# Kernel optimization log

Hardware: AMD Instinct MI355X
Metric: run time of the kernel (lower is better)

The kernel has to match this reference:

```python
import jax, jax.numpy as jnp
import numpy as np
import itertools

N_ELEC = 128
BOX_L = 10.0
DIM = 3
BATCH = 4096


def gen_kpoints(N, L, dim):
    # Faithful numpy port of genKpoints (FermiNet make_kpoints variant).
    rec = 2.0 * np.pi / L
    dk = 1.0 + 1e-05
    max_k = int((N * dk) ** (1.0 / dim) + 0.5)
    ordinals = sorted(range(-max_k, max_k + 1), key=abs)
    ords = np.array(list(itertools.product(ordinals, repeat=dim)), dtype=np.float64)
    kpoints = ords * rec
    order = np.argsort(np.linalg.norm(kpoints, axis=1), kind='stable')
    kpoints = kpoints[order]
    return kpoints[:N].astype(np.float32)


def make_switches(kpoints, dim):
    # Select cos for k-points on the 'positive' side, sin(-k.r) for the rest.
    weights = 10.0 ** np.arange(1, dim + 1)
    weighted_sums = np.sign(kpoints).dot(weights)
    k_signs = np.sign(weighted_sums + 1.0)
    cos_switch = ((k_signs + 1.0) / 2.0).astype(np.float32)
    sin_switch = ((1.0 - k_signs) / 2.0).astype(np.float32)
    return cos_switch, sin_switch


def setup_inputs() -> dict:
    key = jax.random.key(0)
    rs = jax.random.uniform(key, (BATCH, N_ELEC, DIM), dtype=jnp.float32) * BOX_L
    kpoints = gen_kpoints(N_ELEC, BOX_L, DIM)
    cos_switch, sin_switch = make_switches(kpoints, DIM)
    return {
        'rs': rs,
        'kpoints': jnp.asarray(kpoints),
        'cos_switch': jnp.asarray(cos_switch),
        'sin_switch': jnp.asarray(sin_switch),
    }


def reference(rs, kpoints, cos_switch, sin_switch):
    # dots[b, i, m] = k_m . r_{b,i}   -> [B, N, N]
    dots = jnp.einsum('bnd,md->bnm', rs, kpoints)
    # Slater matrix: rows = particles, cols = plane-wave orbitals.
    slater = cos_switch * jnp.cos(dots) + sin_switch * jnp.sin(-dots)
    # log |det| per walker (batched LU) -> [B]
    return jnp.linalg.slogdet(slater)[1]
```

## Files before the change

kernel.cpp:

```cpp
#include <hip/hip_runtime.h>
#include <stdint.h>

#define NM 128
#define NT 512

typedef float v2f __attribute__((ext_vector_type(2)));

__device__ __forceinline__ float readlane_f(float v, int lane) {
    return __int_as_float(__builtin_amdgcn_readlane(__float_as_int(v), lane));
}

__device__ __forceinline__ unsigned wave_max_dpp(unsigned x) {
    int v = (int)x;
#define DPP_STEP(ctrl) \
    { int o = __builtin_amdgcn_update_dpp(0, v, ctrl, 0xf, 0xf, true); \
      v = ((unsigned)o > (unsigned)v) ? o : v; }
    DPP_STEP(0x111)
    DPP_STEP(0x112)
    DPP_STEP(0x114)
    DPP_STEP(0x118)
    DPP_STEP(0x142)
    DPP_STEP(0x143)
#undef DPP_STEP
    return (unsigned)v;
}

__device__ __forceinline__ unsigned pack_key(float v, int r) {
    return (((__float_as_uint(v) & 0x7fffffffu) >> 6) << 7) | (unsigned)r;
}

__device__ __forceinline__ unsigned argmax_bcast(unsigned ka, unsigned kb) {
    const unsigned m = wave_max_dpp(ka > kb ? ka : kb);
    return (unsigned)__builtin_amdgcn_readlane((int)m, 63);
}

__device__ __forceinline__ float sel_readlane(v2f c, int p) {
    return (p < 64) ? readlane_f(c.x, p) : readlane_f(c.y, p - 64);
}

__device__ __forceinline__ void applyBoth(v2f (&sv)[16], int p, v2f lmn) {
    float u[8];
    if (p < 64) {
#pragma unroll
        for (int j = 0; j < 8; ++j) u[j] = readlane_f(sv[j].x, p);
#pragma unroll
        for (int j = 0; j < 8; ++j)
            sv[j] = __builtin_elementwise_fma((v2f){u[j], u[j]}, lmn, sv[j]);
#pragma unroll
        for (int j = 0; j < 8; ++j) u[j] = readlane_f(sv[8 + j].x, p);
#pragma unroll
        for (int j = 0; j < 8; ++j)
            sv[8 + j] = __builtin_elementwise_fma((v2f){u[j], u[j]}, lmn, sv[8 + j]);
    } else {
        const int q = p - 64;
#pragma unroll
        for (int j = 0; j < 8; ++j) u[j] = readlane_f(sv[j].y, q);
#pragma unroll
        for (int j = 0; j < 8; ++j)
            sv[j] = __builtin_elementwise_fma((v2f){u[j], u[j]}, lmn, sv[j]);
#pragma unroll
        for (int j = 0; j < 8; ++j) u[j] = readlane_f(sv[8 + j].y, q);
#pragma unroll
        for (int j = 0; j < 8; ++j)
            sv[8 + j] = __builtin_elementwise_fma((v2f){u[j], u[j]}, lmn, sv[8 + j]);
    }
}

__device__ __forceinline__ void applyHi(v2f (&sv)[16], int p, v2f lmn) {
    float u[8];
    if (p < 64) {
#pragma unroll
        for (int j = 0; j < 8; ++j) u[j] = readlane_f(sv[8 + j].x, p);
#pragma unroll
        for (int j = 0; j < 8; ++j)
            sv[8 + j] = __builtin_elementwise_fma((v2f){u[j], u[j]}, lmn, sv[8 + j]);
    } else {
        const int q = p - 64;
#pragma unroll
        for (int j = 0; j < 8; ++j) u[j] = readlane_f(sv[8 + j].y, q);
#pragma unroll
        for (int j = 0; j < 8; ++j)
            sv[8 + j] = __builtin_elementwise_fma((v2f){u[j], u[j]}, lmn, sv[8 + j]);
    }
}

template<int B>
__device__ __forceinline__ void lookahead8(v2f (&sv)[16], bool& elim0, bool& elim1,
                                           int r0, int r1, int l, int g,
                                           float2 (*colvg)[64],
                                           unsigned* keysF, float* pivsF,
                                           ulonglong2* masks) {
    const bool e0in = elim0, e1in = elim1;
    __builtin_amdgcn_s_setprio(1);
#pragma unroll
    for (int i = 0; i < 8; ++i) {
        const v2f c = sv[B + i];
        const unsigned key = argmax_bcast(elim0 ? 0u : pack_key(c.x, r0),
                                          elim1 ? 0u : pack_key(c.y, r1));
        const int pu = __builtin_amdgcn_readfirstlane((int)(key & 127u));
        const float piv = sel_readlane(c, pu);
        const float rcpn = -__builtin_amdgcn_rcpf(piv);
        elim0 = elim0 || (r0 == pu);
        elim1 = elim1 || (r1 == pu);
        const v2f lmn = { elim0 ? 0.0f : c.x * rcpn,
                          elim1 ? 0.0f : c.y * rcpn };
        colvg[i][l] = make_float2(lmn.x, lmn.y);
        float u[8];
        if (pu < 64) {
#pragma unroll
            for (int m = i + 1; m < 8; ++m) u[m] = readlane_f(sv[B + m].x, pu);
        } else {
#pragma unroll
            for (int m = i + 1; m < 8; ++m) u[m] = readlane_f(sv[B + m].y, pu - 64);
        }
#pragma unroll
        for (int m = i + 1; m < 8; ++m)
            sv[B + m] = __builtin_elementwise_fma((v2f){u[m], u[m]}, lmn, sv[B + m]);
        if (l == 0) { keysF[8 * g + i] = key; pivsF[8 * g + i] = piv; }
    }
    __builtin_amdgcn_s_setprio(0);
    const unsigned long long b0 = __ballot(elim0 && !e0in);
    const unsigned long long b1 = __ballot(elim1 && !e1in);
    if (l == 0) masks[g] = make_ulonglong2(b0, b1);
}

__global__ __launch_bounds__(NT, 8)
void slater_logdet(const float* __restrict__ rs,
                   const float* __restrict__ kpts,
                   const float* __restrict__ csw,
                   const float* __restrict__ ssw,
                   float* __restrict__ out) {
    __shared__ float2 colv[2][8][64];
    __shared__ unsigned keysF[NM];
    __shared__ float    pivsF[NM];
    __shared__ ulonglong2 masks[NM / 8];
    __shared__ float    redf[2];

    const int t  = threadIdx.x;
    const int b  = blockIdx.x;
    const int w  = t >> 6;
    const int l  = t & 63;
    const int r0 = l, r1 = l + 64;

    v2f sv[16];
    {
        const float x0 = rs[(b * NM + r0) * 3 + 0];
        const float y0 = rs[(b * NM + r0) * 3 + 1];
        const float z0 = rs[(b * NM + r0) * 3 + 2];
        const float x1 = rs[(b * NM + r1) * 3 + 0];
        const float y1 = rs[(b * NM + r1) * 3 + 1];
        const float z1 = rs[(b * NM + r1) * 3 + 2];
#pragma unroll
        for (int j = 0; j < 16; ++j) {
            const int m = (j < 8) ? (8 * w + j) : (64 + 8 * w + (j - 8));
            const float kx = kpts[m * 3 + 0], ky = kpts[m * 3 + 1], kz = kpts[m * 3 + 2];
            const float cw = csw[m], sw = ssw[m];
            float sn, cn;
            __sincosf(kx * x0 + ky * y0 + kz * z0, &sn, &cn);
            sv[j].x = cw * cn - sw * sn;
            __sincosf(kx * x1 + ky * y1 + kz * z1, &sn, &cn);
            sv[j].y = cw * cn - sw * sn;
        }
    }

    bool elim0 = false, elim1 = false;

    if (w == 0)
        lookahead8<0>(sv, elim0, elim1, r0, r1, l, 0, colv[0], keysF, pivsF, masks);
    __syncthreads();

    const int liveEnd = w + 7;
    int rd = 0;
    for (; rd <= liveEnd; ++rd) {
        const uint4 ka = *(const uint4*)&keysF[8 * rd];
        const uint4 kb = *(const uint4*)&keysF[8 * rd + 4];
        int p[8];
        p[0] = __builtin_amdgcn_readfirstlane((int)(ka.x & 127u));
        p[1] = __builtin_amdgcn_readfirstlane((int)(ka.y & 127u));
        p[2] = __builtin_amdgcn_readfirstlane((int)(ka.z & 127u));
        p[3] = __builtin_amdgcn_readfirstlane((int)(ka.w & 127u));
        p[4] = __builtin_amdgcn_readfirstlane((int)(kb.x & 127u));
        p[5] = __builtin_amdgcn_readfirstlane((int)(kb.y & 127u));
        p[6] = __builtin_amdgcn_readfirstlane((int)(kb.z & 127u));
        p[7] = __builtin_amdgcn_readfirstlane((int)(kb.w & 127u));
        const ulonglong2 mk = masks[rd];
        elim0 = elim0 || (((mk.x >> l) & 1ull) != 0);
        elim1 = elim1 || (((mk.y >> l) & 1ull) != 0);

        const int par = rd & 1;
        if (rd < w) {
#pragma unroll
            for (int i = 0; i < 8; ++i) {
                const float2 la = colv[par][i][l];
                applyBoth(sv, p[i], (v2f){la.x, la.y});
            }
        } else {
#pragma unroll
            for (int i = 0; i < 8; ++i) {
                const float2 la = colv[par][i][l];
                applyHi(sv, p[i], (v2f){la.x, la.y});
            }
        }

        if (rd == w - 1)
            lookahead8<0>(sv, elim0, elim1, r0, r1, l, rd + 1,
                          colv[(rd + 1) & 1], keysF, pivsF, masks);
        if (rd == w + 7)
            lookahead8<8>(sv, elim0, elim1, r0, r1, l, rd + 1,
                          colv[(rd + 1) & 1], keysF, pivsF, masks);

        __syncthreads();
    }
    for (; rd < 15; ++rd) __syncthreads();

    float lg = 0.0f;
    if (t < NM) {
        lg = __logf(fabsf(pivsF[t]));
#pragma unroll
        for (int off = 32; off > 0; off >>= 1)
            lg += __shfl_xor(lg, off, 64);
        if ((t & 63) == 0) redf[t >> 6] = lg;
    }
    __syncthreads();
    if (t == 0) out[b] = redf[0] + redf[1];
}

extern "C" void kernel_launch(void* const* d_in, const int* in_sizes, int n_in,
                              void* d_out, int out_size, void* d_ws, size_t ws_size,
                              hipStream_t stream) {
    const float* rs = (const float*)d_in[0];
    const float* kp = (const float*)d_in[1];
    const float* cs = (const float*)d_in[2];
    const float* ss = (const float*)d_in[3];
    float* out = (float*)d_out;
    const int batch = in_sizes[0] / (NM * 3);
    slater_logdet<<<dim3(batch), dim3(NT), 0, stream>>>(rs, kp, cs, ss, out);
}
```

Baseline: 342.6 us.

## Run lookahead panel before trailing high-half update and specialize sin/cos setup

In the round just before a wave owns the next panel, the wave now updates only its low columns, immediately factors the lookahead panel at raised priority, and then applies the update to its high columns. This moves the critical-path panel factorization earlier so waiting waves unblock sooner at the barrier. The matrix setup also replaces the sincos-and-blend with a single cos or negated sin chosen by the switch value, which halves transcendental work. That relies on the switches being exact 0/1 complements.

```diff
diff --git a/kernel.cpp b/kernel.cpp
--- a/kernel.cpp
+++ b/kernel.cpp
@@ -38,6 +38,42 @@
     return (p < 64) ? readlane_f(c.x, p) : readlane_f(c.y, p - 64);
 }
 
+__device__ __forceinline__ void applyLo(v2f (&sv)[16], int p, v2f lmn) {
+    float u[8];
+    if (p < 64) {
+#pragma unroll
+        for (int j = 0; j < 8; ++j) u[j] = readlane_f(sv[j].x, p);
+#pragma unroll
+        for (int j = 0; j < 8; ++j)
+            sv[j] = __builtin_elementwise_fma((v2f){u[j], u[j]}, lmn, sv[j]);
+    } else {
+        const int q = p - 64;
+#pragma unroll
+        for (int j = 0; j < 8; ++j) u[j] = readlane_f(sv[j].y, q);
+#pragma unroll
+        for (int j = 0; j < 8; ++j)
+            sv[j] = __builtin_elementwise_fma((v2f){u[j], u[j]}, lmn, sv[j]);
+    }
+}
+
+__device__ __forceinline__ void applyHi(v2f (&sv)[16], int p, v2f lmn) {
+    float u[8];
+    if (p < 64) {
+#pragma unroll
+        for (int j = 0; j < 8; ++j) u[j] = readlane_f(sv[8 + j].x, p);
+#pragma unroll
+        for (int j = 0; j < 8; ++j)
+            sv[8 + j] = __builtin_elementwise_fma((v2f){u[j], u[j]}, lmn, sv[8 + j]);
+    } else {
+        const int q = p - 64;
+#pragma unroll
+        for (int j = 0; j < 8; ++j) u[j] = readlane_f(sv[8 + j].y, q);
+#pragma unroll
+        for (int j = 0; j < 8; ++j)
+            sv[8 + j] = __builtin_elementwise_fma((v2f){u[j], u[j]}, lmn, sv[8 + j]);
+    }
+}
+
 __device__ __forceinline__ void applyBoth(v2f (&sv)[16], int p, v2f lmn) {
     float u[8];
     if (p < 64) {
@@ -58,24 +94,6 @@
 #pragma unroll
         for (int j = 0; j < 8; ++j)
             sv[j] = __builtin_elementwise_fma((v2f){u[j], u[j]}, lmn, sv[j]);
-#pragma unroll
-        for (int j = 0; j < 8; ++j) u[j] = readlane_f(sv[8 + j].y, q);
-#pragma unroll
-        for (int j = 0; j < 8; ++j)
-            sv[8 + j] = __builtin_elementwise_fma((v2f){u[j], u[j]}, lmn, sv[8 + j]);
-    }
-}
-
-__device__ __forceinline__ void applyHi(v2f (&sv)[16], int p, v2f lmn) {
-    float u[8];
-    if (p < 64) {
-#pragma unroll
-        for (int j = 0; j < 8; ++j) u[j] = readlane_f(sv[8 + j].x, p);
-#pragma unroll
-        for (int j = 0; j < 8; ++j)
-            sv[8 + j] = __builtin_elementwise_fma((v2f){u[j], u[j]}, lmn, sv[8 + j]);
-    } else {
-        const int q = p - 64;
 #pragma unroll
         for (int j = 0; j < 8; ++j) u[j] = readlane_f(sv[8 + j].y, q);
 #pragma unroll
@@ -154,12 +172,15 @@
         for (int j = 0; j < 16; ++j) {
             const int m = (j < 8) ? (8 * w + j) : (64 + 8 * w + (j - 8));
             const float kx = kpts[m * 3 + 0], ky = kpts[m * 3 + 1], kz = kpts[m * 3 + 2];
-            const float cw = csw[m], sw = ssw[m];
-            float sn, cn;
-            __sincosf(kx * x0 + ky * y0 + kz * z0, &sn, &cn);
-            sv[j].x = cw * cn - sw * sn;
-            __sincosf(kx * x1 + ky * y1 + kz * z1, &sn, &cn);
-            sv[j].y = cw * cn - sw * sn;
+            const float d0 = kx * x0 + ky * y0 + kz * z0;
+            const float d1 = kx * x1 + ky * y1 + kz * z1;
+            if (csw[m] != 0.0f) {
+                sv[j].x = __cosf(d0);
+                sv[j].y = __cosf(d1);
+            } else {
+                sv[j].x = -__sinf(d0);
+                sv[j].y = -__sinf(d1);
+            }
         }
     }
 
@@ -188,26 +209,37 @@
         elim1 = elim1 || (((mk.y >> l) & 1ull) != 0);
 
         const int par = rd & 1;
-        if (rd < w) {
+        if (rd < w - 1) {
 #pragma unroll
             for (int i = 0; i < 8; ++i) {
                 const float2 la = colv[par][i][l];
                 applyBoth(sv, p[i], (v2f){la.x, la.y});
             }
-        } else {
-#pragma unroll
-            for (int i = 0; i < 8; ++i) {
-                const float2 la = colv[par][i][l];
-                applyHi(sv, p[i], (v2f){la.x, la.y});
-            }
-        }
-
-        if (rd == w - 1)
+        } else if (rd == w - 1) {
+            __builtin_amdgcn_s_setprio(1);
+#pragma unroll
+            for (int i = 0; i < 8; ++i) {
+                const float2 la = colv[par][i][l];
+                applyLo(sv, p[i], (v2f){la.x, la.y});
+            }
             lookahead8<0>(sv, elim0, elim1, r0, r1, l, rd + 1,
                           colv[(rd + 1) & 1], keysF, pivsF, masks);
-        if (rd == w + 7)
-            lookahead8<8>(sv, elim0, elim1, r0, r1, l, rd + 1,
-                          colv[(rd + 1) & 1], keysF, pivsF, masks);
+#pragma unroll
+            for (int i = 0; i < 8; ++i) {
+                const float2 la = colv[par][i][l];
+                applyHi(sv, p[i], (v2f){la.x, la.y});
+            }
+            __builtin_amdgcn_s_setprio(0);
+        } else {
+#pragma unroll
+            for (int i = 0; i < 8; ++i) {
+                const float2 la = colv[par][i][l];
+                applyHi(sv, p[i], (v2f){la.x, la.y});
+            }
+            if (rd == w + 7)
+                lookahead8<8>(sv, elim0, elim1, r0, r1, l, rd + 1,
+                              colv[(rd + 1) & 1], keysF, pivsF, masks);
+        }
 
         __syncthreads();
     }
```

After: 333.9 us (median of 2 runs). 1.03x faster.
